# Performance work log

Hardware: AMD Instinct MI355X
Metric: run time of the kernel (lower is better)

## Reference

```python
import jax, jax.numpy as jnp
import numpy as np

B, N, FN, FE = 8, 256, 64, 64  # batch, nodes, node feat, edge feat


def gnn_layer(A, x, e, We, be, Wn, bn):
    # A: [B,N,N] float mask, x: [B,N,Fn], e: [B,N,N,Fe_in]
    b, n, fn = x.shape
    xi = jnp.broadcast_to(x[:, :, None, :], (b, n, n, fn))  # sender feats
    xj = jnp.broadcast_to(x[:, None, :, :], (b, n, n, fn))  # receiver feats
    h = jnp.concatenate([xi, xj, e], axis=-1)               # [B,N,N,2Fn+Fe]
    e_new = jax.nn.relu(jnp.einsum('bijk,kf->bijf', h, We) + be) * A[..., None]
    deg = jnp.clip(jnp.sum(A, axis=2), 1.0, None)           # [B,N]
    agg = jnp.sum(e_new, axis=2) / deg[..., None]           # mean over neighbors
    x_new = jax.nn.relu(jnp.concatenate([x, agg], axis=-1) @ Wn + bn)
    return x_new, e_new


def setup_inputs() -> dict:
    key = jax.random.key(0)
    ks = jax.random.split(key, 20)
    s = 0.05
    inp = {
        'edge_index': jax.random.randint(ks[0], (B, N, N), 0, 2, dtype=jnp.int32),
        'x': jax.random.normal(ks[1], (B, N, FN), dtype=jnp.float32),
        'edge_attr': jax.random.normal(ks[2], (B, N, N, FE), dtype=jnp.float32),
    }
    # 3 GNN layers: edge-update MLP (2Fn+Fe -> Fe) and node-update (Fn+Fe -> Fn)
    for l in range(3):
        inp[f'We{l}'] = jax.random.normal(ks[3 + 4 * l], (2 * FN + FE, FE), jnp.float32) * s
        inp[f'be{l}'] = jnp.zeros((FE,), jnp.float32)
        inp[f'Wn{l}'] = jax.random.normal(ks[4 + 4 * l], (FN + FE, FN), jnp.float32) * s
        inp[f'bn{l}'] = jnp.zeros((FN,), jnp.float32)
    # spectral-norm MLP head: Fe -> Fe -> Fe -> 1
    inp['W1'] = jax.random.normal(ks[15], (FE, FE), jnp.float32) * s
    inp['b1'] = jnp.zeros((FE,), jnp.float32)
    inp['W2'] = jax.random.normal(ks[16], (FE, FE), jnp.float32) * s
    inp['b2'] = jnp.zeros((FE,), jnp.float32)
    inp['W3'] = jax.random.normal(ks[17], (FE, 1), jnp.float32) * s
    inp['b3'] = jnp.zeros((1,), jnp.float32)
    return inp


def reference(edge_index, x, edge_attr,
              We0, be0, Wn0, bn0,
              We1, be1, Wn1, bn1,
              We2, be2, Wn2, bn2,
              W1, b1, W2, b2, W3, b3):
    A = edge_index.astype(jnp.float32)
    x = x.astype(jnp.float32)
    # layer 0 updates both nodes and edges
    x1, e = gnn_layer(A, x, edge_attr, We0, be0, Wn0, bn0)
    # middle layer(s): node output discarded (as in original forward)
    _, e = gnn_layer(A, x1, e, We1, be1, Wn1, bn1)
    # last layer
    _, edges = gnn_layer(A, x1, e, We2, be2, Wn2, bn2)
    # end == 'edge_mean'
    v = jnp.mean(edges, axis=(1, 2))  # [B, FE]
    h = jax.nn.relu(v @ W1 + b1)
    h = jax.nn.relu(h @ W2 + b2)
    out = h @ W3 + b3                  # [B, 1]
    return jnp.squeeze(out, axis=-1)   # [B]
```

## Files before the change

kernel.cpp:

```cpp
#include <hip/hip_runtime.h>

#define BB 8
#define NN 256
#define FF 64

typedef float f32x4 __attribute__((ext_vector_type(4)));
typedef short s16x8 __attribute__((ext_vector_type(8)));
typedef unsigned short u16;

#define MFMA_BF16(a, b, c) __builtin_amdgcn_mfma_f32_16x16x32_bf16(a, b, c, 0, 0, 0)

__device__ inline u16 f2bf(float x) {
    unsigned u = __float_as_uint(x);
    u += 0x7FFFu + ((u >> 16) & 1u);
    return (u16)(u >> 16);
}
__device__ inline float bf2f(u16 h) { return __uint_as_float(((unsigned)h) << 16); }

__device__ inline s16x8 cvt_a(float4 v0, float4 v1) {
    s16x8 a;
    a[0] = (short)f2bf(v0.x); a[1] = (short)f2bf(v0.y);
    a[2] = (short)f2bf(v0.z); a[3] = (short)f2bf(v0.w);
    a[4] = (short)f2bf(v1.x); a[5] = (short)f2bf(v1.y);
    a[6] = (short)f2bf(v1.z); a[7] = (short)f2bf(v1.w);
    return a;
}

__global__ __launch_bounds__(256) void wprep_kernel(
    const float* __restrict__ We0, const float* __restrict__ We1,
    const float* __restrict__ We2, u16* __restrict__ wimg)
{
    const float* src =
        (blockIdx.x == 0 ? We0 : (blockIdx.x == 1 ? We1 : We2)) + 2 * FF * FF;
    u16* hi = wimg + blockIdx.x * 8192;
    u16* lo = hi + 4096;
    for (int idx = threadIdx.x; idx < 4096; idx += 256) {
        const int f = idx >> 6, rem = idx & 63, cs = rem >> 3, j = rem & 7;
        const int k = ((cs ^ (f & 7)) << 3) | j;
        const float wv = src[k * FF + f];
        const u16 h = f2bf(wv);
        hi[idx] = h;
        lo[idx] = f2bf(wv - bf2f(h));
    }
}

__global__ __launch_bounds__(256) void pq_kernel(
    const float* __restrict__ x, const float* __restrict__ We,
    const float* __restrict__ be, float* __restrict__ P, float* __restrict__ Q,
    float* __restrict__ agg)
{
    const int rl = threadIdx.x >> 6, f = threadIdx.x & 63;
    const int r = blockIdx.x * 4 + rl;
    __shared__ float xs[4][FF];
    xs[rl][f] = x[r * FF + f];
    agg[r * FF + f] = 0.f;
    __syncthreads();
    float p = be[f], q = 0.f;
#pragma unroll
    for (int k = 0; k < FF; ++k) {
        const float xv = xs[rl][k];
        p = fmaf(xv, We[k * FF + f], p);
        q = fmaf(xv, We[(FF + k) * FF + f], q);
    }
    P[r * FF + f] = p;
    Q[r * FF + f] = q;
}

__global__ __launch_bounds__(256, 4) void edge0_kernel(
    const float* e_in, const u16* __restrict__ whi,
    const u16* __restrict__ wlo, const float* __restrict__ P,
    const float* __restrict__ Q, const int* __restrict__ A,
    u16* e1_out, float* __restrict__ agg)
{
    __shared__ u16 Whl[4096], Wll[4096];
    __shared__ u16 Et[8192];
    __shared__ float Al[128], Pl[64];

    const int tid = threadIdx.x;
    const int bt  = blockIdx.x;
    const int bi  = bt >> 1;
    const int b   = bi >> 8;
    const int j0  = (bt & 1) << 7;

#pragma unroll
    for (int m = 0; m < 2; ++m) {
        ((uint4*)Whl)[tid + 256 * m] = ((const uint4*)whi)[tid + 256 * m];
        ((uint4*)Wll)[tid + 256 * m] = ((const uint4*)wlo)[tid + 256 * m];
    }
    if (tid < 128) Al[tid] = (float)A[bi * NN + j0 + tid];
    if (tid < 64)  Pl[tid] = P[bi * FF + tid];

    const int w = tid >> 6, lane = tid & 63;
    const int quad = lane >> 4, l15 = lane & 15, l7 = lane & 7;
    const int e_base = 32 * w;

    const float* erow = e_in + ((size_t)bi * NN + j0) * FF;
    const int*   Arow = A + bi * NN + j0;

    int rm[2];
#pragma unroll
    for (int et = 0; et < 2; ++et) rm[et] = Arow[e_base + et * 16 + l15];

    float al[2][4];
#pragma unroll
    for (int et = 0; et < 2; ++et)
#pragma unroll
        for (int r = 0; r < 4; ++r)
            al[et][r] = (float)Arow[e_base + et * 16 + quad * 4 + r];

    s16x8 afr[2][2];
#pragma unroll
    for (int et = 0; et < 2; ++et) {
        if (rm[et]) {
#pragma unroll
            for (int ks = 0; ks < 2; ++ks) {
                const float* p =
                    erow + (e_base + et * 16 + l15) * FF + ks * 32 + quad * 8;
                afr[ks][et] = cvt_a(*(const float4*)p, *(const float4*)(p + 4));
            }
        } else {
#pragma unroll
            for (int ks = 0; ks < 2; ++ks) afr[ks][et] = (s16x8){0,0,0,0,0,0,0,0};
        }
    }

    float qv[2][4][4];
    const float* Qb = Q + (size_t)b * NN * FF;
#pragma unroll
    for (int et = 0; et < 2; ++et)
#pragma unroll
        for (int ft = 0; ft < 4; ++ft)
#pragma unroll
            for (int r = 0; r < 4; ++r)
                qv[et][ft][r] = (al[et][r] != 0.f)
                    ? Qb[(j0 + e_base + et * 16 + quad * 4 + r) * FF + ft * 16 + l15]
                    : 0.f;

    __syncthreads();

    f32x4 acc[2][4];
#pragma unroll
    for (int et = 0; et < 2; ++et)
#pragma unroll
        for (int ft = 0; ft < 4; ++ft) acc[et][ft] = (f32x4){0.f, 0.f, 0.f, 0.f};

#pragma unroll
    for (int ks = 0; ks < 2; ++ks)
#pragma unroll
        for (int ft = 0; ft < 4; ++ft) {
            const int f  = ft * 16 + l15;
            const int ca = (ks * 4 + quad) ^ l7;
            const s16x8 bh = *(const s16x8*)&Whl[f * 64 + ca * 8];
            const s16x8 bl = *(const s16x8*)&Wll[f * 64 + ca * 8];
#pragma unroll
            for (int et = 0; et < 2; ++et) {
                acc[et][ft] = MFMA_BF16(afr[ks][et], bh, acc[et][ft]);
                acc[et][ft] = MFMA_BF16(afr[ks][et], bl, acc[et][ft]);
            }
        }

    float psum[4] = {0.f, 0.f, 0.f, 0.f};
#pragma unroll
    for (int et = 0; et < 2; ++et)
#pragma unroll
        for (int ft = 0; ft < 4; ++ft)
#pragma unroll
            for (int r = 0; r < 4; ++r) {
                const int el = e_base + et * 16 + quad * 4 + r;
                const int f  = ft * 16 + l15;
                const float val = acc[et][ft][r] + Pl[f] + qv[et][ft][r];
                const float rv  = fmaxf(val, 0.f) * al[et][r];
                Et[el * 64 + f] = f2bf(rv);
                psum[ft] += rv;
            }
#pragma unroll
    for (int ft = 0; ft < 4; ++ft) {
        psum[ft] += __shfl_down(psum[ft], 32);
        psum[ft] += __shfl_down(psum[ft], 16);
    }
    if (lane < 16) {
#pragma unroll
        for (int ft = 0; ft < 4; ++ft)
            atomicAdd(&agg[bi * FF + ft * 16 + l15], psum[ft]);
    }

    __syncthreads();

    u16* dst = e1_out + (size_t)bt * 16384;
#pragma unroll
    for (int m = 0; m < 4; ++m) {
        const int idx = tid + 256 * m;
        const int row = idx >> 3;
        if (Al[row] != 0.f)
            ((uint4*)dst)[idx] = ((const uint4*)Et)[idx];
    }
}

__global__ __launch_bounds__(256) void nodepq_kernel(
    const float* __restrict__ x, const float* __restrict__ agg,
    const int* __restrict__ A,
    const float* __restrict__ Wn, const float* __restrict__ bn,
    const float* __restrict__ We1, const float* __restrict__ be1,
    const float* __restrict__ We2, const float* __restrict__ be2,
    float* __restrict__ P1, float* __restrict__ Q1,
    float* __restrict__ P2, float* __restrict__ Q2, float* __restrict__ v)
{
    const int rl = threadIdx.x >> 6, f = threadIdx.x & 63;
    const int r = blockIdx.x * 4 + rl;
    __shared__ float s[4][2 * FF];
    __shared__ float x1s[4][FF];

    float da = (float)A[r * NN + f] + (float)A[r * NN + f + 64] +
               (float)A[r * NN + f + 128] + (float)A[r * NN + f + 192];
#pragma unroll
    for (int off = 32; off > 0; off >>= 1) da += __shfl_down(da, off, 64);
    const float deg = fmaxf(__shfl(da, 0, 64), 1.0f);

    s[rl][f]      = x[r * FF + f];
    s[rl][FF + f] = agg[r * FF + f] / deg;
    if (blockIdx.x == 0) {
        v[threadIdx.x] = 0.f;
        v[256 + threadIdx.x] = 0.f;
    }
    __syncthreads();
    float a = bn[f];
#pragma unroll
    for (int k = 0; k < 2 * FF; ++k) a = fmaf(s[rl][k], Wn[k * FF + f], a);
    x1s[rl][f] = fmaxf(a, 0.f);
    __syncthreads();
    float p1 = be1[f], q1 = 0.f, p2 = be2[f], q2 = 0.f;
#pragma unroll
    for (int k = 0; k < FF; ++k) {
        const float xv = x1s[rl][k];
        p1 = fmaf(xv, We1[k * FF + f], p1);
        q1 = fmaf(xv, We1[(FF + k) * FF + f], q1);
        p2 = fmaf(xv, We2[k * FF + f], p2);
        q2 = fmaf(xv, We2[(FF + k) * FF + f], q2);
    }
    P1[r * FF + f] = p1;  Q1[r * FF + f] = q1;
    P2[r * FF + f] = p2;  Q2[r * FF + f] = q2;
}

__global__ __launch_bounds__(256, 4) void edge12_kernel(
    const u16* __restrict__ e1,
    const u16* __restrict__ w1hi, const u16* __restrict__ w1lo,
    const u16* __restrict__ w2hi, const u16* __restrict__ w2lo,
    const float* __restrict__ P1, const float* __restrict__ Q1,
    const float* __restrict__ P2, const float* __restrict__ Q2,
    const int* __restrict__ A, float* __restrict__ v)
{
    __shared__ u16 Wh[4096], Wl[4096];
    __shared__ u16 E2[128 * 64];
    __shared__ float Pl1[64], Pl2[64], red[64];

    const int tid = threadIdx.x;
    const int bt  = blockIdx.x;
    const int bi  = bt >> 1;
    const int b   = bi >> 8;
    const int j0  = (bt & 1) << 7;

    const uint4 w2h0 = ((const uint4*)w2hi)[tid];
    const uint4 w2h1 = ((const uint4*)w2hi)[tid + 256];
    const uint4 w2l0 = ((const uint4*)w2lo)[tid];
    const uint4 w2l1 = ((const uint4*)w2lo)[tid + 256];

#pragma unroll
    for (int m = 0; m < 2; ++m) {
        ((uint4*)Wh)[tid + 256 * m] = ((const uint4*)w1hi)[tid + 256 * m];
        ((uint4*)Wl)[tid + 256 * m] = ((const uint4*)w1lo)[tid + 256 * m];
    }
    if (tid < 64) {
        Pl1[tid] = P1[bi * FF + tid];
        Pl2[tid] = P2[bi * FF + tid];
        red[tid] = 0.f;
    }

    const int w = tid >> 6, lane = tid & 63;
    const int quad = lane >> 4, l15 = lane & 15, l7 = lane & 7;
    const int e_base = 32 * w;

    const int* Arow = A + bi * NN + j0;

    int rm[2];
#pragma unroll
    for (int et = 0; et < 2; ++et) rm[et] = Arow[e_base + et * 16 + l15];

    float al[2][4];
#pragma unroll
    for (int et = 0; et < 2; ++et)
#pragma unroll
        for (int r = 0; r < 4; ++r)
            al[et][r] = (float)Arow[e_base + et * 16 + quad * 4 + r];

    const u16* etile = e1 + (size_t)bt * 16384;
    s16x8 afr[2][2];
#pragma unroll
    for (int et = 0; et < 2; ++et) {
        if (rm[et]) {
#pragma unroll
            for (int ks = 0; ks < 2; ++ks)
                afr[ks][et] = *(const s16x8*)
                    &etile[(e_base + et * 16 + l15) * 64 + ks * 32 + quad * 8];
        } else {
#pragma unroll
            for (int ks = 0; ks < 2; ++ks) afr[ks][et] = (s16x8){0,0,0,0,0,0,0,0};
        }
    }

    float qv[2][4][4];
    {
        const float* Qb = Q1 + (size_t)b * NN * FF;
#pragma unroll
        for (int et = 0; et < 2; ++et)
#pragma unroll
            for (int ft = 0; ft < 4; ++ft)
#pragma unroll
                for (int r = 0; r < 4; ++r)
                    qv[et][ft][r] = (al[et][r] != 0.f)
                        ? Qb[(j0 + e_base + et * 16 + quad * 4 + r) * FF + ft * 16 + l15]
                        : 0.f;
    }

    __syncthreads();

    f32x4 acc[2][4];
#pragma unroll
    for (int et = 0; et < 2; ++et)
#pragma unroll
        for (int ft = 0; ft < 4; ++ft) acc[et][ft] = (f32x4){0.f, 0.f, 0.f, 0.f};

#pragma unroll
    for (int ks = 0; ks < 2; ++ks)
#pragma unroll
        for (int ft = 0; ft < 4; ++ft) {
            const int f  = ft * 16 + l15;
            const int ca = (ks * 4 + quad) ^ l7;
            const s16x8 bh = *(const s16x8*)&Wh[f * 64 + ca * 8];
            const s16x8 bl = *(const s16x8*)&Wl[f * 64 + ca * 8];
#pragma unroll
            for (int et = 0; et < 2; ++et) {
                acc[et][ft] = MFMA_BF16(afr[ks][et], bh, acc[et][ft]);
                acc[et][ft] = MFMA_BF16(afr[ks][et], bl, acc[et][ft]);
            }
        }

#pragma unroll
    for (int et = 0; et < 2; ++et)
#pragma unroll
        for (int ft = 0; ft < 4; ++ft)
#pragma unroll
            for (int r = 0; r < 4; ++r) {
                const int el = e_base + et * 16 + quad * 4 + r;
                const int f  = ft * 16 + l15;
                const float val = acc[et][ft][r] + Pl1[f] + qv[et][ft][r];
                const float rv  = fmaxf(val, 0.f) * al[et][r];
                const int c  = f >> 3;
                const int cs = c ^ (el & 7);
                E2[el * 64 + cs * 8 + l7] = f2bf(rv);
            }

    {
        const float* Qb = Q2 + (size_t)b * NN * FF;
#pragma unroll
        for (int et = 0; et < 2; ++et)
#pragma unroll
            for (int ft = 0; ft < 4; ++ft)
#pragma unroll
                for (int r = 0; r < 4; ++r)
                    qv[et][ft][r] = (al[et][r] != 0.f)
                        ? Qb[(j0 + e_base + et * 16 + quad * 4 + r) * FF + ft * 16 + l15]
                        : 0.f;
    }

    __syncthreads();

    ((uint4*)Wh)[tid]       = w2h0;
    ((uint4*)Wh)[tid + 256] = w2h1;
    ((uint4*)Wl)[tid]       = w2l0;
    ((uint4*)Wl)[tid + 256] = w2l1;

    __syncthreads();

#pragma unroll
    for (int et = 0; et < 2; ++et)
#pragma unroll
        for (int ft = 0; ft < 4; ++ft) acc[et][ft] = (f32x4){0.f, 0.f, 0.f, 0.f};

#pragma unroll
    for (int ks = 0; ks < 2; ++ks) {
        s16x8 a2[2];
#pragma unroll
        for (int et = 0; et < 2; ++et) {
            const int e  = e_base + et * 16 + l15;
            const int ca = (ks * 4 + quad) ^ l7;
            a2[et] = *(const s16x8*)&E2[e * 64 + ca * 8];
        }
#pragma unroll
        for (int ft = 0; ft < 4; ++ft) {
            const int f  = ft * 16 + l15;
            const int ca = (ks * 4 + quad) ^ l7;
            const s16x8 bh = *(const s16x8*)&Wh[f * 64 + ca * 8];
            const s16x8 bl = *(const s16x8*)&Wl[f * 64 + ca * 8];
#pragma unroll
            for (int et = 0; et < 2; ++et) {
                acc[et][ft] = MFMA_BF16(a2[et], bh, acc[et][ft]);
                acc[et][ft] = MFMA_BF16(a2[et], bl, acc[et][ft]);
            }
        }
    }

    float psum[4] = {0.f, 0.f, 0.f, 0.f};
#pragma unroll
    for (int et = 0; et < 2; ++et)
#pragma unroll
        for (int ft = 0; ft < 4; ++ft)
#pragma unroll
            for (int r = 0; r < 4; ++r) {
                const float val = acc[et][ft][r] + Pl2[ft * 16 + l15] + qv[et][ft][r];
                psum[ft] += fmaxf(val, 0.f) * al[et][r];
            }
#pragma unroll
    for (int ft = 0; ft < 4; ++ft) {
        psum[ft] += __shfl_down(psum[ft], 32);
        psum[ft] += __shfl_down(psum[ft], 16);
    }
    if (lane < 16) {
#pragma unroll
        for (int ft = 0; ft < 4; ++ft)
            atomicAdd(&red[ft * 16 + l15], psum[ft]);
    }
    __syncthreads();
    if (tid < 64) atomicAdd(&v[b * FF + tid], red[tid]);
}

__global__ __launch_bounds__(64) void head_kernel(
    const float* __restrict__ vsum, const float* __restrict__ W1,
    const float* __restrict__ b1, const float* __restrict__ W2,
    const float* __restrict__ b2, const float* __restrict__ W3,
    const float* __restrict__ b3, float* __restrict__ out)
{
    const int f = threadIdx.x;
    __shared__ float hv[BB][FF];
    __shared__ float h1[BB][FF];
#pragma unroll
    for (int b = 0; b < BB; ++b) hv[b][f] = vsum[b * FF + f] * (1.0f / 65536.0f);
    __syncthreads();
#pragma unroll
    for (int b = 0; b < BB; ++b) {
        float acc = b1[f];
#pragma unroll
        for (int k = 0; k < FF; ++k) acc = fmaf(hv[b][k], W1[k * FF + f], acc);
        h1[b][f] = fmaxf(acc, 0.f);
    }
    __syncthreads();
#pragma unroll
    for (int b = 0; b < BB; ++b) {
        float acc = b2[f];
#pragma unroll
        for (int k = 0; k < FF; ++k) acc = fmaf(h1[b][k], W2[k * FF + f], acc);
        hv[b][f] = fmaxf(acc, 0.f);
    }
    __syncthreads();
#pragma unroll
    for (int b = 0; b < BB; ++b) {
        float p = hv[b][f] * W3[f];
#pragma unroll
        for (int off = 32; off > 0; off >>= 1) p += __shfl_down(p, off);
        if (f == 0) out[b] = p + b3[0];
    }
}

extern "C" void kernel_launch(void* const* d_in, const int* in_sizes, int n_in,
                              void* d_out, int out_size, void* d_ws, size_t ws_size,
                              hipStream_t stream)
{
    const int*   A      = (const int*)d_in[0];
    const float* x      = (const float*)d_in[1];
    float*       e_attr = (float*)d_in[2];

    const float* We0 = (const float*)d_in[3];
    const float* be0 = (const float*)d_in[4];
    const float* Wn0 = (const float*)d_in[5];
    const float* bn0 = (const float*)d_in[6];
    const float* We1 = (const float*)d_in[7];
    const float* be1 = (const float*)d_in[8];
    const float* We2 = (const float*)d_in[11];
    const float* be2 = (const float*)d_in[12];
    const float* W1 = (const float*)d_in[15];
    const float* b1 = (const float*)d_in[16];
    const float* W2 = (const float*)d_in[17];
    const float* b2 = (const float*)d_in[18];
    const float* W3 = (const float*)d_in[19];
    const float* b3 = (const float*)d_in[20];
    float* out = (float*)d_out;
    (void)in_sizes; (void)n_in; (void)out_size; (void)ws_size;

    const int R = BB * NN;
    float* P1  = (float*)d_ws;
    float* Q1  = P1 + R * FF;
    float* P2  = Q1 + R * FF;
    float* Q2  = P2 + R * FF;
    float* agg = Q2 + R * FF;
    float* v   = agg + R * FF;
    u16*  wimg = (u16*)(v + 512);

    const int EB = 2 * R;

    wprep_kernel<<<3, 256, 0, stream>>>(We0, We1, We2, wimg);
    pq_kernel<<<R / 4, 256, 0, stream>>>(x, We0, be0, P1, Q1, agg);
    edge0_kernel<<<EB, 256, 0, stream>>>(e_attr, wimg, wimg + 4096, P1, Q1, A,
                                         (u16*)e_attr, agg);
    nodepq_kernel<<<R / 4, 256, 0, stream>>>(x, agg, A, Wn0, bn0, We1, be1,
                                             We2, be2, P1, Q1, P2, Q2, v);
    edge12_kernel<<<EB, 256, 0, stream>>>((const u16*)e_attr,
                                          wimg + 8192, wimg + 12288,
                                          wimg + 16384, wimg + 20480,
                                          P1, Q1, P2, Q2, A, v);
    head_kernel<<<1, 64, 0, stream>>>(v, W1, b1, W2, b2, W3, b3, out);
}
```

Before: 335.8 us.

## Process full edge row per 512-thread block with LDS aggregation

```diff
diff --git a/kernel.cpp b/kernel.cpp
--- a/kernel.cpp
+++ b/kernel.cpp
@@ -66,36 +66,31 @@
     Q[r * FF + f] = q;
 }
 
-__global__ __launch_bounds__(256, 4) void edge0_kernel(
+__global__ __launch_bounds__(512, 6) void edge0_kernel(
     const float* e_in, const u16* __restrict__ whi,
     const u16* __restrict__ wlo, const float* __restrict__ P,
     const float* __restrict__ Q, const int* __restrict__ A,
     u16* e1_out, float* __restrict__ agg)
 {
     __shared__ u16 Whl[4096], Wll[4096];
-    __shared__ u16 Et[8192];
-    __shared__ float Al[128], Pl[64];
+    __shared__ u16 Et[NN * FF];
+    __shared__ float Al[NN], Pl[64], aggred[64];
 
     const int tid = threadIdx.x;
-    const int bt  = blockIdx.x;
-    const int bi  = bt >> 1;
+    const int bi  = blockIdx.x;
     const int b   = bi >> 8;
-    const int j0  = (bt & 1) << 7;
-
-#pragma unroll
-    for (int m = 0; m < 2; ++m) {
-        ((uint4*)Whl)[tid + 256 * m] = ((const uint4*)whi)[tid + 256 * m];
-        ((uint4*)Wll)[tid + 256 * m] = ((const uint4*)wlo)[tid + 256 * m];
-    }
-    if (tid < 128) Al[tid] = (float)A[bi * NN + j0 + tid];
-    if (tid < 64)  Pl[tid] = P[bi * FF + tid];
+
+    ((uint4*)Whl)[tid] = ((const uint4*)whi)[tid];
+    ((uint4*)Wll)[tid] = ((const uint4*)wlo)[tid];
+    if (tid < NN) Al[tid] = (float)A[bi * NN + tid];
+    if (tid < 64) { Pl[tid] = P[bi * FF + tid]; aggred[tid] = 0.f; }
 
     const int w = tid >> 6, lane = tid & 63;
     const int quad = lane >> 4, l15 = lane & 15, l7 = lane & 7;
     const int e_base = 32 * w;
 
-    const float* erow = e_in + ((size_t)bi * NN + j0) * FF;
-    const int*   Arow = A + bi * NN + j0;
+    const float* erow = e_in + (size_t)bi * NN * FF;
+    const int*   Arow = A + bi * NN;
 
     int rm[2];
 #pragma unroll
@@ -133,7 +128,7 @@
 #pragma unroll
             for (int r = 0; r < 4; ++r)
                 qv[et][ft][r] = (al[et][r] != 0.f)
-                    ? Qb[(j0 + e_base + et * 16 + quad * 4 + r) * FF + ft * 16 + l15]
+                    ? Qb[(e_base + et * 16 + quad * 4 + r) * FF + ft * 16 + l15]
                     : 0.f;
 
     __syncthreads();
@@ -181,15 +176,17 @@
     if (lane < 16) {
 #pragma unroll
         for (int ft = 0; ft < 4; ++ft)
-            atomicAdd(&agg[bi * FF + ft * 16 + l15], psum[ft]);
-    }
-
-    __syncthreads();
-
-    u16* dst = e1_out + (size_t)bt * 16384;
+            atomicAdd(&aggred[ft * 16 + l15], psum[ft]);
+    }
+
+    __syncthreads();
+
+    if (tid < 64) agg[bi * FF + tid] = aggred[tid];
+
+    u16* dst = e1_out + (size_t)bi * (NN * FF);
 #pragma unroll
     for (int m = 0; m < 4; ++m) {
-        const int idx = tid + 256 * m;
+        const int idx = tid + 512 * m;
         const int row = idx >> 3;
         if (Al[row] != 0.f)
             ((uint4*)dst)[idx] = ((const uint4*)Et)[idx];
@@ -241,7 +238,7 @@
     P2[r * FF + f] = p2;  Q2[r * FF + f] = q2;
 }
 
-__global__ __launch_bounds__(256, 4) void edge12_kernel(
+__global__ __launch_bounds__(512, 6) void edge12_kernel(
     const u16* __restrict__ e1,
     const u16* __restrict__ w1hi, const u16* __restrict__ w1lo,
     const u16* __restrict__ w2hi, const u16* __restrict__ w2lo,
@@ -250,25 +247,18 @@
     const int* __restrict__ A, float* __restrict__ v)
 {
     __shared__ u16 Wh[4096], Wl[4096];
-    __shared__ u16 E2[128 * 64];
+    __shared__ u16 E2[NN * FF];
     __shared__ float Pl1[64], Pl2[64], red[64];
 
     const int tid = threadIdx.x;
-    const int bt  = blockIdx.x;
-    const int bi  = bt >> 1;
+    const int bi  = blockIdx.x;
     const int b   = bi >> 8;
-    const int j0  = (bt & 1) << 7;
 
     const uint4 w2h0 = ((const uint4*)w2hi)[tid];
-    const uint4 w2h1 = ((const uint4*)w2hi)[tid + 256];
     const uint4 w2l0 = ((const uint4*)w2lo)[tid];
-    const uint4 w2l1 = ((const uint4*)w2lo)[tid + 256];
-
-#pragma unroll
-    for (int m = 0; m < 2; ++m) {
-        ((uint4*)Wh)[tid + 256 * m] = ((const uint4*)w1hi)[tid + 256 * m];
-        ((uint4*)Wl)[tid + 256 * m] = ((const uint4*)w1lo)[tid + 256 * m];
-    }
+
+    ((uint4*)Wh)[tid] = ((const uint4*)w1hi)[tid];
+    ((uint4*)Wl)[tid] = ((const uint4*)w1lo)[tid];
     if (tid < 64) {
         Pl1[tid] = P1[bi * FF + tid];
         Pl2[tid] = P2[bi * FF + tid];
@@ -279,7 +269,7 @@
     const int quad = lane >> 4, l15 = lane & 15, l7 = lane & 7;
     const int e_base = 32 * w;
 
-    const int* Arow = A + bi * NN + j0;
+    const int* Arow = A + bi * NN;
 
     int rm[2];
 #pragma unroll
@@ -292,7 +282,7 @@
         for (int r = 0; r < 4; ++r)
             al[et][r] = (float)Arow[e_base + et * 16 + quad * 4 + r];
 
-    const u16* etile = e1 + (size_t)bt * 16384;
+    const u16* etile = e1 + (size_t)bi * (NN * FF);
     s16x8 afr[2][2];
 #pragma unroll
     for (int et = 0; et < 2; ++et) {
@@ -317,7 +307,7 @@
 #pragma unroll
                 for (int r = 0; r < 4; ++r)
                     qv[et][ft][r] = (al[et][r] != 0.f)
-                        ? Qb[(j0 + e_base + et * 16 + quad * 4 + r) * FF + ft * 16 + l15]
+                        ? Qb[(e_base + et * 16 + quad * 4 + r) * FF + ft * 16 + l15]
                         : 0.f;
     }
 
@@ -368,16 +358,14 @@
 #pragma unroll
                 for (int r = 0; r < 4; ++r)
                     qv[et][ft][r] = (al[et][r] != 0.f)
-                        ? Qb[(j0 + e_base + et * 16 + quad * 4 + r) * FF + ft * 16 + l15]
+                        ? Qb[(e_base + et * 16 + quad * 4 + r) * FF + ft * 16 + l15]
                         : 0.f;
     }
 
     __syncthreads();
 
-    ((uint4*)Wh)[tid]       = w2h0;
-    ((uint4*)Wh)[tid + 256] = w2h1;
-    ((uint4*)Wl)[tid]       = w2l0;
-    ((uint4*)Wl)[tid + 256] = w2l1;
+    ((uint4*)Wh)[tid] = w2h0;
+    ((uint4*)Wl)[tid] = w2l0;
 
     __syncthreads();
 
@@ -504,17 +492,15 @@
     float* v   = agg + R * FF;
     u16*  wimg = (u16*)(v + 512);
 
-    const int EB = 2 * R;
-
     wprep_kernel<<<3, 256, 0, stream>>>(We0, We1, We2, wimg);
     pq_kernel<<<R / 4, 256, 0, stream>>>(x, We0, be0, P1, Q1, agg);
-    edge0_kernel<<<EB, 256, 0, stream>>>(e_attr, wimg, wimg + 4096, P1, Q1, A,
-                                         (u16*)e_attr, agg);
+    edge0_kernel<<<R, 512, 0, stream>>>(e_attr, wimg, wimg + 4096, P1, Q1, A,
+                                        (u16*)e_attr, agg);
     nodepq_kernel<<<R / 4, 256, 0, stream>>>(x, agg, A, Wn0, bn0, We1, be1,
                                              We2, be2, P1, Q1, P2, Q2, v);
-    edge12_kernel<<<EB, 256, 0, stream>>>((const u16*)e_attr,
-                                          wimg + 8192, wimg + 12288,
-                                          wimg + 16384, wimg + 20480,
-                                          P1, Q1, P2, Q2, A, v);
+    edge12_kernel<<<R, 512, 0, stream>>>((const u16*)e_attr,
+                                         wimg + 8192, wimg + 12288,
+                                         wimg + 16384, wimg + 20480,
+                                         P1, Q1, P2, Q2, A, v);
     head_kernel<<<1, 64, 0, stream>>>(v, W1, b1, W2, b2, W3, b3, out);
 }
```

After: 389.3 us. 15.9% more time.

## Store Q transposed for vectorized float4 loads and drop per-edge mask branches

Applied to the files above, without the earlier changes.

```diff
diff --git a/kernel.cpp b/kernel.cpp
--- a/kernel.cpp
+++ b/kernel.cpp
@@ -46,7 +46,7 @@
 
 __global__ __launch_bounds__(256) void pq_kernel(
     const float* __restrict__ x, const float* __restrict__ We,
-    const float* __restrict__ be, float* __restrict__ P, float* __restrict__ Q,
+    const float* __restrict__ be, float* __restrict__ P, float* __restrict__ QT,
     float* __restrict__ agg)
 {
     const int rl = threadIdx.x >> 6, f = threadIdx.x & 63;
@@ -63,18 +63,18 @@
         q = fmaf(xv, We[(FF + k) * FF + f], q);
     }
     P[r * FF + f] = p;
-    Q[r * FF + f] = q;
+    QT[((r >> 8) * FF + f) * NN + (r & 255)] = q;
 }
 
 __global__ __launch_bounds__(256, 4) void edge0_kernel(
     const float* e_in, const u16* __restrict__ whi,
     const u16* __restrict__ wlo, const float* __restrict__ P,
-    const float* __restrict__ Q, const int* __restrict__ A,
+    const float* __restrict__ QT0, const int* __restrict__ A,
     u16* e1_out, float* __restrict__ agg)
 {
     __shared__ u16 Whl[4096], Wll[4096];
     __shared__ u16 Et[8192];
-    __shared__ float Al[128], Pl[64];
+    __shared__ float Pl[64];
 
     const int tid = threadIdx.x;
     const int bt  = blockIdx.x;
@@ -87,8 +87,7 @@
         ((uint4*)Whl)[tid + 256 * m] = ((const uint4*)whi)[tid + 256 * m];
         ((uint4*)Wll)[tid + 256 * m] = ((const uint4*)wlo)[tid + 256 * m];
     }
-    if (tid < 128) Al[tid] = (float)A[bi * NN + j0 + tid];
-    if (tid < 64)  Pl[tid] = P[bi * FF + tid];
+    if (tid < 64) Pl[tid] = P[bi * FF + tid];
 
     const int w = tid >> 6, lane = tid & 63;
     const int quad = lane >> 4, l15 = lane & 15, l7 = lane & 7;
@@ -125,16 +124,18 @@
     }
 
     float qv[2][4][4];
-    const float* Qb = Q + (size_t)b * NN * FF;
-#pragma unroll
-    for (int et = 0; et < 2; ++et)
-#pragma unroll
-        for (int ft = 0; ft < 4; ++ft)
-#pragma unroll
-            for (int r = 0; r < 4; ++r)
-                qv[et][ft][r] = (al[et][r] != 0.f)
-                    ? Qb[(j0 + e_base + et * 16 + quad * 4 + r) * FF + ft * 16 + l15]
-                    : 0.f;
+    {
+        const float* QTb = QT0 + (size_t)b * FF * NN;
+#pragma unroll
+        for (int et = 0; et < 2; ++et)
+#pragma unroll
+            for (int ft = 0; ft < 4; ++ft) {
+                const float4 t = *(const float4*)
+                    &QTb[(ft * 16 + l15) * NN + j0 + e_base + et * 16 + quad * 4];
+                qv[et][ft][0] = t.x; qv[et][ft][1] = t.y;
+                qv[et][ft][2] = t.z; qv[et][ft][3] = t.w;
+            }
+    }
 
     __syncthreads();
 
@@ -188,12 +189,8 @@
 
     u16* dst = e1_out + (size_t)bt * 16384;
 #pragma unroll
-    for (int m = 0; m < 4; ++m) {
-        const int idx = tid + 256 * m;
-        const int row = idx >> 3;
-        if (Al[row] != 0.f)
-            ((uint4*)dst)[idx] = ((const uint4*)Et)[idx];
-    }
+    for (int m = 0; m < 4; ++m)
+        ((uint4*)dst)[tid + 256 * m] = ((const uint4*)Et)[tid + 256 * m];
 }
 
 __global__ __launch_bounds__(256) void nodepq_kernel(
@@ -202,8 +199,8 @@
     const float* __restrict__ Wn, const float* __restrict__ bn,
     const float* __restrict__ We1, const float* __restrict__ be1,
     const float* __restrict__ We2, const float* __restrict__ be2,
-    float* __restrict__ P1, float* __restrict__ Q1,
-    float* __restrict__ P2, float* __restrict__ Q2, float* __restrict__ v)
+    float* __restrict__ P1, float* __restrict__ QT1,
+    float* __restrict__ P2, float* __restrict__ QT2, float* __restrict__ v)
 {
     const int rl = threadIdx.x >> 6, f = threadIdx.x & 63;
     const int r = blockIdx.x * 4 + rl;
@@ -237,16 +234,19 @@
         p2 = fmaf(xv, We2[k * FF + f], p2);
         q2 = fmaf(xv, We2[(FF + k) * FF + f], q2);
     }
-    P1[r * FF + f] = p1;  Q1[r * FF + f] = q1;
-    P2[r * FF + f] = p2;  Q2[r * FF + f] = q2;
+    P1[r * FF + f] = p1;
+    P2[r * FF + f] = p2;
+    const int qt = ((r >> 8) * FF + f) * NN + (r & 255);
+    QT1[qt] = q1;
+    QT2[qt] = q2;
 }
 
 __global__ __launch_bounds__(256, 4) void edge12_kernel(
     const u16* __restrict__ e1,
     const u16* __restrict__ w1hi, const u16* __restrict__ w1lo,
     const u16* __restrict__ w2hi, const u16* __restrict__ w2lo,
-    const float* __restrict__ P1, const float* __restrict__ Q1,
-    const float* __restrict__ P2, const float* __restrict__ Q2,
+    const float* __restrict__ P1, const float* __restrict__ QT1,
+    const float* __restrict__ P2, const float* __restrict__ QT2,
     const int* __restrict__ A, float* __restrict__ v)
 {
     __shared__ u16 Wh[4096], Wl[4096];
@@ -281,10 +281,6 @@
 
     const int* Arow = A + bi * NN + j0;
 
-    int rm[2];
-#pragma unroll
-    for (int et = 0; et < 2; ++et) rm[et] = Arow[e_base + et * 16 + l15];
-
     float al[2][4];
 #pragma unroll
     for (int et = 0; et < 2; ++et)
@@ -295,30 +291,24 @@
     const u16* etile = e1 + (size_t)bt * 16384;
     s16x8 afr[2][2];
 #pragma unroll
-    for (int et = 0; et < 2; ++et) {
-        if (rm[et]) {
-#pragma unroll
-            for (int ks = 0; ks < 2; ++ks)
-                afr[ks][et] = *(const s16x8*)
-                    &etile[(e_base + et * 16 + l15) * 64 + ks * 32 + quad * 8];
-        } else {
-#pragma unroll
-            for (int ks = 0; ks < 2; ++ks) afr[ks][et] = (s16x8){0,0,0,0,0,0,0,0};
-        }
-    }
+    for (int ks = 0; ks < 2; ++ks)
+#pragma unroll
+        for (int et = 0; et < 2; ++et)
+            afr[ks][et] = *(const s16x8*)
+                &etile[(e_base + et * 16 + l15) * 64 + ks * 32 + quad * 8];
 
     float qv[2][4][4];
     {
-        const float* Qb = Q1 + (size_t)b * NN * FF;
+        const float* QTb = QT1 + (size_t)b * FF * NN;
 #pragma unroll
         for (int et = 0; et < 2; ++et)
 #pragma unroll
-            for (int ft = 0; ft < 4; ++ft)
-#pragma unroll
-                for (int r = 0; r < 4; ++r)
-                    qv[et][ft][r] = (al[et][r] != 0.f)
-                        ? Qb[(j0 + e_base + et * 16 + quad * 4 + r) * FF + ft * 16 + l15]
-                        : 0.f;
+            for (int ft = 0; ft < 4; ++ft) {
+                const float4 t = *(const float4*)
+                    &QTb[(ft * 16 + l15) * NN + j0 + e_base + et * 16 + quad * 4];
+                qv[et][ft][0] = t.x; qv[et][ft][1] = t.y;
+                qv[et][ft][2] = t.z; qv[et][ft][3] = t.w;
+            }
     }
 
     __syncthreads();
@@ -360,16 +350,16 @@
             }
 
     {
-        const float* Qb = Q2 + (size_t)b * NN * FF;
+        const float* QTb = QT2 + (size_t)b * FF * NN;
 #pragma unroll
         for (int et = 0; et < 2; ++et)
 #pragma unroll
-            for (int ft = 0; ft < 4; ++ft)
-#pragma unroll
-                for (int r = 0; r < 4; ++r)
-                    qv[et][ft][r] = (al[et][r] != 0.f)
-                        ? Qb[(j0 + e_base + et * 16 + quad * 4 + r) * FF + ft * 16 + l15]
-                        : 0.f;
+            for (int ft = 0; ft < 4; ++ft) {
+                const float4 t = *(const float4*)
+                    &QTb[(ft * 16 + l15) * NN + j0 + e_base + et * 16 + quad * 4];
+                qv[et][ft][0] = t.x; qv[et][ft][1] = t.y;
+                qv[et][ft][2] = t.z; qv[et][ft][3] = t.w;
+            }
     }
 
     __syncthreads();
@@ -496,25 +486,27 @@
     (void)in_sizes; (void)n_in; (void)out_size; (void)ws_size;
 
     const int R = BB * NN;
-    float* P1  = (float*)d_ws;
-    float* Q1  = P1 + R * FF;
-    float* P2  = Q1 + R * FF;
-    float* Q2  = P2 + R * FF;
-    float* agg = Q2 + R * FF;
+    float* P0  = (float*)d_ws;
+    float* QT0 = P0 + R * FF;
+    float* P1  = QT0 + R * FF;
+    float* QT1 = P1 + R * FF;
+    float* P2  = QT1 + R * FF;
+    float* QT2 = P2 + R * FF;
+    float* agg = QT2 + R * FF;
     float* v   = agg + R * FF;
     u16*  wimg = (u16*)(v + 512);
 
     const int EB = 2 * R;
 
     wprep_kernel<<<3, 256, 0, stream>>>(We0, We1, We2, wimg);
-    pq_kernel<<<R / 4, 256, 0, stream>>>(x, We0, be0, P1, Q1, agg);
-    edge0_kernel<<<EB, 256, 0, stream>>>(e_attr, wimg, wimg + 4096, P1, Q1, A,
+    pq_kernel<<<R / 4, 256, 0, stream>>>(x, We0, be0, P0, QT0, agg);
+    edge0_kernel<<<EB, 256, 0, stream>>>(e_attr, wimg, wimg + 4096, P0, QT0, A,
                                          (u16*)e_attr, agg);
     nodepq_kernel<<<R / 4, 256, 0, stream>>>(x, agg, A, Wn0, bn0, We1, be1,
-                                             We2, be2, P1, Q1, P2, Q2, v);
+                                             We2, be2, P1, QT1, P2, QT2, v);
     edge12_kernel<<<EB, 256, 0, stream>>>((const u16*)e_attr,
                                           wimg + 8192, wimg + 12288,
                                           wimg + 16384, wimg + 20480,
-                                          P1, Q1, P2, Q2, A, v);
+                                          P1, QT1, P2, QT2, A, v);
     head_kernel<<<1, 64, 0, stream>>>(v, W1, b1, W2, b2, W3, b3, out);
 }
```

Result: slower. 353.2 us (+5.2%).
